# Optimization experiments

Hardware: AMD Instinct MI355X
Metric: run time of the kernel (lower is better)

Reference implementation:

```python
import jax, jax.numpy as jnp
import numpy as np

DIM = 33          # LUT lattice size per color axis
B, H, W = 4, 2048, 2048


def setup_inputs() -> dict:
    key = jax.random.key(0)
    k1, k2 = jax.random.split(key)
    # pixel values in [0, 1) index the LUT lattice
    x = jax.random.uniform(k1, (B, 3, H, W), dtype=jnp.float32)
    # module initializes LUT to zeros; use small random values so the
    # interpolation (and its gradient) is non-trivial for testing
    LUT = 0.1 * jax.random.normal(k2, (3, DIM, DIM, DIM), dtype=jnp.float32)
    return {"x": x, "LUT": LUT}


def _trilinear_lut(LUT, x):
    """Trilinear 3D LUT interpolation (image-adaptive-3DLUT trilinear op).

    LUT: (3, D, D, D) indexed as LUT[c, b_idx, g_idx, r_idx]
    x:   (B, 3, H, W) RGB in [0, 1]
    returns (B, 3, H, W)
    """
    D = LUT.shape[1]
    bins = D - 1  # number of cells per axis (binsize = 1/bins)
    rr = x[:, 0] * bins  # (B, H, W) continuous lattice coords
    gg = x[:, 1] * bins
    bb = x[:, 2] * bins
    r0 = jnp.clip(jnp.floor(rr).astype(jnp.int32), 0, bins - 1)
    g0 = jnp.clip(jnp.floor(gg).astype(jnp.int32), 0, bins - 1)
    b0 = jnp.clip(jnp.floor(bb).astype(jnp.int32), 0, bins - 1)
    fr = rr - r0  # fractional offsets within the cell
    fg = gg - g0
    fb = bb - b0

    acc = jnp.zeros((3,) + r0.shape, dtype=LUT.dtype)  # (3, B, H, W)
    for db in (0, 1):
        wb = fb if db else (1.0 - fb)
        for dg in (0, 1):
            wg = fg if dg else (1.0 - fg)
            for dr in (0, 1):
                wr = fr if dr else (1.0 - fr)
                w = (wb * wg * wr)[None]                     # (1, B, H, W)
                acc = acc + w * LUT[:, b0 + db, g0 + dg, r0 + dr]
    return jnp.transpose(acc, (1, 0, 2, 3))  # (B, 3, H, W)


def reference(x, LUT):
    return _trilinear_lut(LUT, x)
```

## Files before the change

kernel.cpp:

```cpp
#include <hip/hip_runtime.h>

#define DIMK 33
#define D2   (DIMK * DIMK)
#define D3   (DIMK * DIMK * DIMK)
#define NVPAD 35940
#define HWPIX (2048 * 2048)
#define HWSHIFT 22

typedef float        f32x4 __attribute__((ext_vector_type(4)));
typedef unsigned int u32;
typedef u32          u32x4 __attribute__((ext_vector_type(4)));

#define QTAB_OFF_BYTES 256

__global__ __launch_bounds__(256) void k_absmax(const float* __restrict__ LUT,
                                                u32* __restrict__ ws) {
    int t = blockIdx.x * 256 + threadIdx.x;
    float m = 0.0f;
    for (int i = t; i < 3 * D3; i += (int)gridDim.x * 256)
        m = fmaxf(m, fabsf(LUT[i]));
    for (int off = 32; off; off >>= 1)
        m = fmaxf(m, __shfl_down(m, off, 64));
    if ((threadIdx.x & 63) == 0)
        atomicMax(ws, __float_as_uint(m));
}

__global__ __launch_bounds__(256) void k_quant(const float* __restrict__ LUT,
                                               const u32* __restrict__ ws,
                                               u32* __restrict__ qtab) {
    int t = blockIdx.x * 256 + threadIdx.x;
    if (t >= D3) return;
    float s = __uint_as_float(*ws);
    s = fmaxf(s, 1e-20f);
    float inv = 511.0f / s;
    u32 w = 0;
#pragma unroll
    for (int c = 0; c < 3; ++c) {
        float v = LUT[c * D3 + t];
        int q = (int)rintf(v * inv);
        q = max(-511, min(511, q));
        w |= ((u32)(q + 512)) << (10 * c);
    }
    qtab[t] = w;
}

__global__ __launch_bounds__(1024, 4) void k_apply(const float* __restrict__ x,
                                                   const u32* __restrict__ qtab,
                                                   const u32* __restrict__ ws,
                                                   float* __restrict__ out,
                                                   int nquads) {
    __shared__ u32 tab[NVPAD];
    {
        u32x4* dst = (u32x4*)tab;
        const u32x4* src = (const u32x4*)qtab;
        for (int i = threadIdx.x; i < NVPAD / 4; i += 1024)
            dst[i] = src[i];
    }
    float s511 = __uint_as_float(*ws) * (1.0f / 511.0f);
    float bias = 512.0f * s511;
    __syncthreads();

    int stride = (int)gridDim.x * 1024;
    for (int t = blockIdx.x * 1024 + threadIdx.x; t < nquads; t += stride) {
        int p = t << 2;
        int b = p >> HWSHIFT;
        int o = p & (HWPIX - 1);
        const float* xb = x + (size_t)b * 3 * HWPIX + o;

        f32x4 r4 = __builtin_nontemporal_load((const f32x4*)(xb));
        f32x4 g4 = __builtin_nontemporal_load((const f32x4*)(xb + HWPIX));
        f32x4 b4 = __builtin_nontemporal_load((const f32x4*)(xb + 2 * HWPIX));

        f32x4 oc0, oc1, oc2;
#pragma unroll
        for (int i = 0; i < 4; ++i) {
            float fr = r4[i] * 32.0f;
            float fg = g4[i] * 32.0f;
            float fb = b4[i] * 32.0f;
            int ri = (int)fr;
            int gi = (int)fg;
            int bi = (int)fb;
            ri = max(0, min(31, ri));
            gi = max(0, min(31, gi));
            bi = max(0, min(31, bi));
            fr -= (float)ri;
            fg -= (float)gi;
            fb -= (float)bi;

            int vid = bi * D2 + gi * DIMK + ri;
            u32 c000 = tab[vid];
            u32 c001 = tab[vid + 1];
            u32 c010 = tab[vid + DIMK];
            u32 c011 = tab[vid + DIMK + 1];
            u32 c100 = tab[vid + D2];
            u32 c101 = tab[vid + D2 + 1];
            u32 c110 = tab[vid + D2 + DIMK];
            u32 c111 = tab[vid + D2 + DIMK + 1];

            float wr0 = 1.0f - fr, wg0 = 1.0f - fg, wb0 = 1.0f - fb;
            float wbg00 = wb0 * wg0, wbg01 = wb0 * fg;
            float wbg10 = fb * wg0, wbg11 = fb * fg;

            float A0 = 0.f, A1 = 0.f, A2 = 0.f;
            auto acc = [&](u32 cw, float w) {
                A0 += w * (float)(cw & 1023u);
                A1 += w * (float)((cw >> 10) & 1023u);
                A2 += w * (float)((cw >> 20) & 1023u);
            };
            acc(c000, wbg00 * wr0);
            acc(c001, wbg00 * fr);
            acc(c010, wbg01 * wr0);
            acc(c011, wbg01 * fr);
            acc(c100, wbg10 * wr0);
            acc(c101, wbg10 * fr);
            acc(c110, wbg11 * wr0);
            acc(c111, wbg11 * fr);

            oc0[i] = A0 * s511 - bias;
            oc1[i] = A1 * s511 - bias;
            oc2[i] = A2 * s511 - bias;
        }

        float* ob = out + (size_t)b * 3 * HWPIX + o;
        __builtin_nontemporal_store(oc0, (f32x4*)(ob));
        __builtin_nontemporal_store(oc1, (f32x4*)(ob + HWPIX));
        __builtin_nontemporal_store(oc2, (f32x4*)(ob + 2 * HWPIX));
    }
}

__global__ __launch_bounds__(256) void lut_apply_direct(const float* __restrict__ x,
                                                        const float* __restrict__ LUT,
                                                        float* __restrict__ out,
                                                        int nquads) {
    int t = blockIdx.x * blockDim.x + threadIdx.x;
    if (t >= nquads) return;
    int p = t << 2;
    int b = p >> HWSHIFT;
    int o = p & (HWPIX - 1);
    const float* xb = x + (size_t)b * 3 * HWPIX + o;

    f32x4 r4 = *(const f32x4*)(xb);
    f32x4 g4 = *(const f32x4*)(xb + HWPIX);
    f32x4 b4 = *(const f32x4*)(xb + 2 * HWPIX);
    f32x4 oc0, oc1, oc2;

#pragma unroll
    for (int i = 0; i < 4; ++i) {
        float fr = r4[i] * 32.0f;
        float fg = g4[i] * 32.0f;
        float fb = b4[i] * 32.0f;
        int ri = max(0, min(31, (int)fr));
        int gi = max(0, min(31, (int)fg));
        int bi = max(0, min(31, (int)fb));
        fr -= (float)ri;
        fg -= (float)gi;
        fb -= (float)bi;

        float wr1[2] = {1.0f - fr, fr};
        float wg1[2] = {1.0f - fg, fg};
        float wb1[2] = {1.0f - fb, fb};
        float a0 = 0.f, a1 = 0.f, a2 = 0.f;
#pragma unroll
        for (int db = 0; db < 2; ++db)
#pragma unroll
            for (int dg = 0; dg < 2; ++dg)
#pragma unroll
                for (int dr = 0; dr < 2; ++dr) {
                    float w = wb1[db] * wg1[dg] * wr1[dr];
                    int idx = (bi + db) * D2 + (gi + dg) * DIMK + (ri + dr);
                    a0 += w * LUT[idx];
                    a1 += w * LUT[D3 + idx];
                    a2 += w * LUT[2 * D3 + idx];
                }
        oc0[i] = a0;
        oc1[i] = a1;
        oc2[i] = a2;
    }
    float* ob = out + (size_t)b * 3 * HWPIX + o;
    *(f32x4*)(ob) = oc0;
    *(f32x4*)(ob + HWPIX) = oc1;
    *(f32x4*)(ob + 2 * HWPIX) = oc2;
}

extern "C" void kernel_launch(void* const* d_in, const int* in_sizes, int n_in,
                              void* d_out, int out_size, void* d_ws, size_t ws_size,
                              hipStream_t stream) {
    const float* x   = (const float*)d_in[0];
    const float* LUT = (const float*)d_in[1];
    float* out = (float*)d_out;

    int npix   = in_sizes[0] / 3;
    int nquads = npix >> 2;

    const size_t need = QTAB_OFF_BYTES + (size_t)NVPAD * 4;
    if (ws_size >= need) {
        u32* scale = (u32*)d_ws;
        u32* qtab  = (u32*)((char*)d_ws + QTAB_OFF_BYTES);
        hipMemsetAsync(scale, 0, 4, stream);
        k_absmax<<<128, 256, 0, stream>>>(LUT, scale);
        k_quant<<<(D3 + 255) / 256, 256, 0, stream>>>(LUT, scale, qtab);
        k_apply<<<1024, 1024, 0, stream>>>(x, qtab, scale, out, nquads);
    } else {
        int blocks = (nquads + 255) / 256;
        lut_apply_direct<<<blocks, 256, 0, stream>>>(x, LUT, out, nquads);
    }
}
```

Before: 421.0 us.

## Prefetch next pixel quad in registers and batch LDS gathers in apply kernel

The apply kernel now issues the first iteration's global loads before the LUT is copied into shared memory. Inside the grid-stride loop it also loads the next quad's inputs while processing the current one, so HBM latency overlaps the table fill and the interpolation math. All 32 shared-memory gathers for the four pixels are issued together before the accumulation, and output stores change from nontemporal to plain stores. The cost is more live registers, which could reduce occupancy under the 1024-thread launch bound, and the plain stores may pollute caches.

```diff
diff --git a/kernel.cpp b/kernel.cpp
--- a/kernel.cpp
+++ b/kernel.cpp
@@ -50,6 +50,21 @@
                                                    float* __restrict__ out,
                                                    int nquads) {
     __shared__ u32 tab[NVPAD];
+
+    const int stride = (int)gridDim.x * 1024;
+    int t = blockIdx.x * 1024 + threadIdx.x;
+
+    f32x4 r4 = {0.f, 0.f, 0.f, 0.f}, g4 = r4, b4 = r4;
+    if (t < nquads) {
+        int p = t << 2;
+        int b = p >> HWSHIFT;
+        int o = p & (HWPIX - 1);
+        const float* xb = x + (size_t)b * 3 * HWPIX + o;
+        r4 = __builtin_nontemporal_load((const f32x4*)(xb));
+        g4 = __builtin_nontemporal_load((const f32x4*)(xb + HWPIX));
+        b4 = __builtin_nontemporal_load((const f32x4*)(xb + 2 * HWPIX));
+    }
+
     {
         u32x4* dst = (u32x4*)tab;
         const u32x4* src = (const u32x4*)qtab;
@@ -60,71 +75,84 @@
     float bias = 512.0f * s511;
     __syncthreads();
 
-    int stride = (int)gridDim.x * 1024;
-    for (int t = blockIdx.x * 1024 + threadIdx.x; t < nquads; t += stride) {
-        int p = t << 2;
-        int b = p >> HWSHIFT;
-        int o = p & (HWPIX - 1);
-        const float* xb = x + (size_t)b * 3 * HWPIX + o;
-
-        f32x4 r4 = __builtin_nontemporal_load((const f32x4*)(xb));
-        f32x4 g4 = __builtin_nontemporal_load((const f32x4*)(xb + HWPIX));
-        f32x4 b4 = __builtin_nontemporal_load((const f32x4*)(xb + 2 * HWPIX));
+    while (t < nquads) {
+        int tn = t + stride;
+        f32x4 nr = {0.f, 0.f, 0.f, 0.f}, ng = nr, nb = nr;
+        if (tn < nquads) {
+            int pn = tn << 2;
+            int bn = pn >> HWSHIFT;
+            int on = pn & (HWPIX - 1);
+            const float* xbn = x + (size_t)bn * 3 * HWPIX + on;
+            nr = __builtin_nontemporal_load((const f32x4*)(xbn));
+            ng = __builtin_nontemporal_load((const f32x4*)(xbn + HWPIX));
+            nb = __builtin_nontemporal_load((const f32x4*)(xbn + 2 * HWPIX));
+        }
+
+        int  vid[4];
+        float fr[4], fg[4], fb[4];
+#pragma unroll
+        for (int i = 0; i < 4; ++i) {
+            float cr = r4[i] * 32.0f;
+            float cg = g4[i] * 32.0f;
+            float cb = b4[i] * 32.0f;
+            int ri = max(0, min(31, (int)cr));
+            int gi = max(0, min(31, (int)cg));
+            int bi = max(0, min(31, (int)cb));
+            fr[i] = cr - (float)ri;
+            fg[i] = cg - (float)gi;
+            fb[i] = cb - (float)bi;
+            vid[i] = bi * D2 + gi * DIMK + ri;
+        }
+
+        u32 cw[4][8];
+#pragma unroll
+        for (int i = 0; i < 4; ++i) {
+            int v = vid[i];
+            cw[i][0] = tab[v];
+            cw[i][1] = tab[v + 1];
+            cw[i][2] = tab[v + DIMK];
+            cw[i][3] = tab[v + DIMK + 1];
+            cw[i][4] = tab[v + D2];
+            cw[i][5] = tab[v + D2 + 1];
+            cw[i][6] = tab[v + D2 + DIMK];
+            cw[i][7] = tab[v + D2 + DIMK + 1];
+        }
 
         f32x4 oc0, oc1, oc2;
 #pragma unroll
         for (int i = 0; i < 4; ++i) {
-            float fr = r4[i] * 32.0f;
-            float fg = g4[i] * 32.0f;
-            float fb = b4[i] * 32.0f;
-            int ri = (int)fr;
-            int gi = (int)fg;
-            int bi = (int)fb;
-            ri = max(0, min(31, ri));
-            gi = max(0, min(31, gi));
-            bi = max(0, min(31, bi));
-            fr -= (float)ri;
-            fg -= (float)gi;
-            fb -= (float)bi;
-
-            int vid = bi * D2 + gi * DIMK + ri;
-            u32 c000 = tab[vid];
-            u32 c001 = tab[vid + 1];
-            u32 c010 = tab[vid + DIMK];
-            u32 c011 = tab[vid + DIMK + 1];
-            u32 c100 = tab[vid + D2];
-            u32 c101 = tab[vid + D2 + 1];
-            u32 c110 = tab[vid + D2 + DIMK];
-            u32 c111 = tab[vid + D2 + DIMK + 1];
-
-            float wr0 = 1.0f - fr, wg0 = 1.0f - fg, wb0 = 1.0f - fb;
-            float wbg00 = wb0 * wg0, wbg01 = wb0 * fg;
-            float wbg10 = fb * wg0, wbg11 = fb * fg;
-
+            float wr0 = 1.0f - fr[i], wg0 = 1.0f - fg[i], wb0 = 1.0f - fb[i];
+            float wbg00 = wb0 * wg0, wbg01 = wb0 * fg[i];
+            float wbg10 = fb[i] * wg0, wbg11 = fb[i] * fg[i];
+            float w[8] = {wbg00 * wr0, wbg00 * fr[i], wbg01 * wr0, wbg01 * fr[i],
+                          wbg10 * wr0, wbg10 * fr[i], wbg11 * wr0, wbg11 * fr[i]};
             float A0 = 0.f, A1 = 0.f, A2 = 0.f;
-            auto acc = [&](u32 cw, float w) {
-                A0 += w * (float)(cw & 1023u);
-                A1 += w * (float)((cw >> 10) & 1023u);
-                A2 += w * (float)((cw >> 20) & 1023u);
-            };
-            acc(c000, wbg00 * wr0);
-            acc(c001, wbg00 * fr);
-            acc(c010, wbg01 * wr0);
-            acc(c011, wbg01 * fr);
-            acc(c100, wbg10 * wr0);
-            acc(c101, wbg10 * fr);
-            acc(c110, wbg11 * wr0);
-            acc(c111, wbg11 * fr);
-
+#pragma unroll
+            for (int cn = 0; cn < 8; ++cn) {
+                u32 c = cw[i][cn];
+                A0 += w[cn] * (float)(c & 1023u);
+                A1 += w[cn] * (float)((c >> 10) & 1023u);
+                A2 += w[cn] * (float)((c >> 20) & 1023u);
+            }
             oc0[i] = A0 * s511 - bias;
             oc1[i] = A1 * s511 - bias;
             oc2[i] = A2 * s511 - bias;
         }
 
-        float* ob = out + (size_t)b * 3 * HWPIX + o;
-        __builtin_nontemporal_store(oc0, (f32x4*)(ob));
-        __builtin_nontemporal_store(oc1, (f32x4*)(ob + HWPIX));
-        __builtin_nontemporal_store(oc2, (f32x4*)(ob + 2 * HWPIX));
+        {
+            int p = t << 2;
+            int b = p >> HWSHIFT;
+            int o = p & (HWPIX - 1);
+            float* ob = out + (size_t)b * 3 * HWPIX + o;
+            *(f32x4*)(ob) = oc0;
+            *(f32x4*)(ob + HWPIX) = oc1;
+            *(f32x4*)(ob + 2 * HWPIX) = oc2;
+        }
+
+        t = tn;
+        r4 = nr;
+        g4 = ng;
+        b4 = nb;
     }
 }
 
```

Result: faster. 350.1 us (-16.8%).
